# Performance work log

Hardware: AMD Instinct MI355X
Metric: run time of the kernel (lower is better)

The kernel has to match this reference:

```python
import jax, jax.numpy as jnp
import numpy as np

HEAD_SIZE = 128
B, T = 16, 2048

def setup_inputs() -> dict:
    key = jax.random.key(0)
    x = jax.random.normal(key, (B, T, 3 * HEAD_SIZE), dtype=jnp.float32)
    return {"x": x}

def reference(x) -> jnp.ndarray:
    # x: [B, T, 3*head_size] -> split into k, q, v (this order matches torch split)
    k, q, v = jnp.split(x, 3, axis=-1)  # each [B, T, D]
    d = k.shape[-1]
    scale = d ** -0.5
    # scores: [B, T, T]
    wei = jnp.einsum('bqd,bkd->bqk', q, k) * scale
    Tq = x.shape[1]
    causal = jnp.tril(jnp.ones((Tq, Tq), dtype=bool))
    wei = jnp.where(causal, wei, -jnp.inf)
    wei = jax.nn.softmax(wei, axis=-1)
    out = jnp.einsum('bqk,bkd->bqd', wei, v)  # [B, T, D]
    return out
```

## Files before the change

### kernel.cpp

```cpp
#include <hip/hip_runtime.h>

#define SEQ_T 2048
#define HDIM  128
#define NB    16
#define NTILES (SEQ_T / 64)
#define TILE_SHORTS 8192

typedef __attribute__((ext_vector_type(8))) short short8;
typedef __attribute__((ext_vector_type(4))) float float4v;
typedef __attribute__((ext_vector_type(4))) unsigned int uint4v;

#define EXP2F(x) __builtin_amdgcn_exp2f(x)

__device__ __forceinline__ unsigned int bfpack2(float a, float b) {
  unsigned int ua = __builtin_bit_cast(unsigned int, a);
  unsigned int ub = __builtin_bit_cast(unsigned int, b);
  return ((ua + 0x8000u) >> 16) | ((ub + 0x8000u) & 0xFFFF0000u);
}
__device__ __forceinline__ unsigned short f2bf(float a) {
  return (unsigned short)((__builtin_bit_cast(unsigned int, a) + 0x8000u) >> 16);
}
__device__ __forceinline__ float bf2f(unsigned short h) {
  unsigned int u = ((unsigned int)h) << 16;
  return __builtin_bit_cast(float, u);
}

__device__ __forceinline__ float dpp_max16(float x) {
  int t;
  t = __builtin_amdgcn_mov_dpp(__builtin_bit_cast(int, x), 0xB1, 0xF, 0xF, true);
  x = fmaxf(x, __builtin_bit_cast(float, t));
  t = __builtin_amdgcn_mov_dpp(__builtin_bit_cast(int, x), 0x4E, 0xF, 0xF, true);
  x = fmaxf(x, __builtin_bit_cast(float, t));
  t = __builtin_amdgcn_mov_dpp(__builtin_bit_cast(int, x), 0x141, 0xF, 0xF, true);
  x = fmaxf(x, __builtin_bit_cast(float, t));
  t = __builtin_amdgcn_mov_dpp(__builtin_bit_cast(int, x), 0x140, 0xF, 0xF, true);
  x = fmaxf(x, __builtin_bit_cast(float, t));
  return x;
}
__device__ __forceinline__ float dpp_sum16(float x) {
  int t;
  t = __builtin_amdgcn_mov_dpp(__builtin_bit_cast(int, x), 0xB1, 0xF, 0xF, true);
  x += __builtin_bit_cast(float, t);
  t = __builtin_amdgcn_mov_dpp(__builtin_bit_cast(int, x), 0x4E, 0xF, 0xF, true);
  x += __builtin_bit_cast(float, t);
  t = __builtin_amdgcn_mov_dpp(__builtin_bit_cast(int, x), 0x141, 0xF, 0xF, true);
  x += __builtin_bit_cast(float, t);
  t = __builtin_amdgcn_mov_dpp(__builtin_bit_cast(int, x), 0x140, 0xF, 0xF, true);
  x += __builtin_bit_cast(float, t);
  return x;
}

template<int CS> struct ChunkCfg;
template<> struct ChunkCfg<4> { static const int CPB = 72, SPB = 70, QB0 = 2; };
template<> struct ChunkCfg<8> { static const int CPB = 40, SPB = 36, QB0 = 4; };

__global__ __launch_bounds__(256) void prepass2(const float* __restrict__ x,
                                                unsigned short* __restrict__ kbuf,
                                                unsigned short* __restrict__ vbuf) {
  const int b = blockIdx.x >> 5;
  const int t = blockIdx.x & 31;
  const int tid = threadIdx.x;
  __shared__ __align__(16) unsigned short Klds[8192];
  __shared__ __align__(16) unsigned short Vlds[8192];

  const float* xb = x + (size_t)b * (SEQ_T * 384) + (size_t)t * 64 * 384;

  for (int i = 0; i < 8; ++i) {
    int idx = tid + i * 256;
    int row = idx >> 5, c4 = (idx & 31) << 2;
    float4v f = *(const float4v*)(xb + (size_t)row * 384 + c4);
    *(uint2*)&Klds[row * 128 + c4] = make_uint2(bfpack2(f[0], f[1]), bfpack2(f[2], f[3]));
  }
  {
    int kb = tid >> 5, db = tid & 31;
    for (int p = 0; p < 2; ++p) {
      int kbx = kb + p * 8;
      const float* vb = xb + (size_t)(4 * kbx) * 384 + 256 + 4 * db;
      float4v v0 = *(const float4v*)(vb);
      float4v v1 = *(const float4v*)(vb + 384);
      float4v v2 = *(const float4v*)(vb + 768);
      float4v v3 = *(const float4v*)(vb + 1152);
      int u = kbx >> 1, o = (kbx & 1) * 4;
      for (int j = 0; j < 4; ++j) {
        int d = 4 * db + j;
        *(uint2*)&Vlds[d * 64 + ((u + d) & 7) * 8 + o] =
            make_uint2(bfpack2(v0[j], v1[j]), bfpack2(v2[j], v3[j]));
      }
    }
  }
  __syncthreads();

  unsigned short* kdst = kbuf + (size_t)blockIdx.x * TILE_SHORTS;
  unsigned short* vdst = vbuf + (size_t)blockIdx.x * TILE_SHORTS;
  for (int i = 0; i < 4; ++i) {
    int n = tid + i * 256;
    int r = n >> 4, pu = n & 15, u = (pu - r) & 15;
    *(uint4v*)&kdst[n * 8] = *(const uint4v*)&Klds[r * 128 + u * 8];
    *(uint4v*)&vdst[n * 8] = *(const uint4v*)&Vlds[n * 8];
  }
}

template<int CS>
__global__ __launch_bounds__(512, 4) void attn_chunk_k(const float* __restrict__ x,
                                                       const unsigned short* __restrict__ kbuf,
                                                       const unsigned short* __restrict__ vbuf,
                                                       unsigned short* __restrict__ Opart,
                                                       float* __restrict__ mlpart,
                                                       float* __restrict__ out) {
  const int f = blockIdx.x;
  const int b = f / ChunkCfg<CS>::CPB;
  const int c = f - b * ChunkCfg<CS>::CPB;
  int qb = 0, cum = 0;
  for (;;) {
    int gg = (2 * qb + 2 + CS - 1) / CS;
    if (c < cum + gg) break;
    cum += gg; ++qb;
  }
  const int g = (2 * qb + 2 + CS - 1) / CS;
  const int k = c - cum;
  const int sBeg = k * CS;
  const int sEnd = min(sBeg + CS, 2 * qb + 2);

  const int tid  = threadIdx.x;
  const int qt   = tid >> 6;
  const int lane = tid & 63;
  const int low  = lane & 15;
  const int quad = lane >> 4;
  const int q0   = qb * 128 + qt * 16;

  __shared__ __align__(16) unsigned char smem[40960];
  unsigned short* Ks = (unsigned short*)smem;
  unsigned short* Vt = (unsigned short*)(smem + 16384);
  unsigned short* Ps = (unsigned short*)(smem + 32768);

  const float* xb = x + (size_t)b * (SEQ_T * 3 * HDIM);
  const unsigned short* kt = kbuf + (size_t)b * NTILES * TILE_SHORTS;
  const unsigned short* vt = vbuf + (size_t)b * NTILES * TILE_SHORTS;

  const float qs = 0.08838834764831845f * 1.4426950408889634f;
  short8 qa[4];
  {
    const float* qrow = xb + (size_t)(q0 + low) * 384 + 128;
    for (int kc = 0; kc < 4; ++kc) {
      float4v f0 = *(const float4v*)(qrow + kc * 32 + quad * 8);
      float4v f1 = *(const float4v*)(qrow + kc * 32 + quad * 8 + 4);
      uint4v u = { bfpack2(f0[0] * qs, f0[1] * qs), bfpack2(f0[2] * qs, f0[3] * qs),
                   bfpack2(f1[0] * qs, f1[1] * qs), bfpack2(f1[2] * qs, f1[3] * qs) };
      qa[kc] = __builtin_bit_cast(short8, u);
    }
  }

  float4v accv[8];
  for (int i = 0; i < 8; ++i) accv[i] = (float4v){0.f, 0.f, 0.f, 0.f};
  float l_i[4] = {0.f, 0.f, 0.f, 0.f};

  const int ch = qt * 2;

  uint4v kr0, kr1, vr0, vr1;
  {
    const unsigned short* ksrc = kt + (size_t)sBeg * TILE_SHORTS;
    const unsigned short* vsrc = vt + (size_t)sBeg * TILE_SHORTS;
    kr0 = *(const uint4v*)(ksrc + (size_t)ch * 512 + lane * 8);
    kr1 = *(const uint4v*)(ksrc + (size_t)(ch + 1) * 512 + lane * 8);
    vr0 = *(const uint4v*)(vsrc + (size_t)ch * 512 + lane * 8);
    vr1 = *(const uint4v*)(vsrc + (size_t)(ch + 1) * 512 + lane * 8);
  }

  for (int s = sBeg; s < sEnd; ++s) {
    __syncthreads();

    *(uint4v*)&Ks[(size_t)ch * 512 + lane * 8]       = kr0;
    *(uint4v*)&Ks[(size_t)(ch + 1) * 512 + lane * 8] = kr1;
    *(uint4v*)&Vt[(size_t)ch * 512 + lane * 8]       = vr0;
    *(uint4v*)&Vt[(size_t)(ch + 1) * 512 + lane * 8] = vr1;

    __syncthreads();

    if (s + 1 < sEnd) {
      const unsigned short* ksrc = kt + (size_t)(s + 1) * TILE_SHORTS;
      const unsigned short* vsrc = vt + (size_t)(s + 1) * TILE_SHORTS;
      kr0 = *(const uint4v*)(ksrc + (size_t)ch * 512 + lane * 8);
      kr1 = *(const uint4v*)(ksrc + (size_t)(ch + 1) * 512 + lane * 8);
      vr0 = *(const uint4v*)(vsrc + (size_t)ch * 512 + lane * 8);
      vr1 = *(const uint4v*)(vsrc + (size_t)(ch + 1) * 512 + lane * 8);
    }

    for (int h = 0; h < 2; ++h) {
      const int c0 = s * 64 + h * 32;
      if (c0 > q0 + 15) continue;
      const int Ra = (h << 5) + low;
      const int Rb = Ra + 16;
      float4v s0 = {0.f,0.f,0.f,0.f}, s1 = {0.f,0.f,0.f,0.f};
      for (int kc = 0; kc < 4; ++kc) {
        short8 kf0 = *(const short8*)&Ks[Ra * 128 + (((kc * 4 + quad) + Ra) & 15) * 8];
        short8 kf1 = *(const short8*)&Ks[Rb * 128 + (((kc * 4 + quad) + Rb) & 15) * 8];
        s0 = __builtin_amdgcn_mfma_f32_16x16x32_bf16(qa[kc], kf0, s0, 0, 0, 0);
        s1 = __builtin_amdgcn_mfma_f32_16x16x32_bf16(qa[kc], kf1, s1, 0, 0, 0);
      }
      if (c0 + 31 > q0) {
        for (int r = 0; r < 4; ++r) {
          int qrow = q0 + quad * 4 + r;
          s0[r] = (c0 + low      <= qrow) ? s0[r] : -1e30f;
          s1[r] = (c0 + 16 + low <= qrow) ? s1[r] : -1e30f;
        }
      }
      for (int r = 0; r < 4; ++r) {
        s0[r] = EXP2F(s0[r]);
        s1[r] = EXP2F(s1[r]);
      }
      for (int r = 0; r < 4; ++r) l_i[r] += s0[r] + s1[r];

      unsigned short* pw = Ps + qt * 512;
      for (int r = 0; r < 4; ++r) {
        int row = quad * 4 + r;
        pw[row * 32 + low]      = f2bf(s0[r]);
        pw[row * 32 + 16 + low] = f2bf(s1[r]);
      }
      short8 pa = *(const short8*)&pw[low * 32 + quad * 8];

      const int ub = (h << 2) + quad;
      for (int nt = 0; nt < 8; ++nt) {
        int d = nt * 16 + low;
        short8 vf = *(const short8*)&Vt[d * 64 + ((ub + d) & 7) * 8];
        accv[nt] = __builtin_amdgcn_mfma_f32_16x16x32_bf16(pa, vf, accv[nt], 0, 0, 0);
      }
    }
  }

  for (int r = 0; r < 4; ++r) l_i[r] = dpp_sum16(l_i[r]);

  if (g == 1) {
    float inv[4];
    for (int r = 0; r < 4; ++r) inv[r] = 1.f / l_i[r];
    float* ob = out + ((size_t)b * SEQ_T + q0) * HDIM;
    for (int nt = 0; nt < 8; ++nt)
      for (int r = 0; r < 4; ++r)
        ob[(size_t)(quad * 4 + r) * HDIM + nt * 16 + low] = accv[nt][r] * inv[r];
  } else {
    const int slot = b * ChunkCfg<CS>::SPB + (cum - ChunkCfg<CS>::QB0) + k;
    unsigned short* op = Opart + (size_t)slot * 16384 + (size_t)qt * 16 * 128;
    for (int nt = 0; nt < 8; ++nt)
      for (int r = 0; r < 4; ++r)
        op[(size_t)(quad * 4 + r) * 128 + nt * 16 + low] = f2bf(accv[nt][r]);
    if (low == 0) {
      float* ml = mlpart + (size_t)slot * 256;
      for (int r = 0; r < 4; ++r)
        ml[qt * 16 + quad * 4 + r] = l_i[r];
    }
  }
}

template<int CS>
__global__ __launch_bounds__(256) void merge_k(const unsigned short* __restrict__ Opart,
                                               const float* __restrict__ mlpart,
                                               float* __restrict__ out) {
  const int QB0 = ChunkCfg<CS>::QB0;
  const int rowsPB = (16 - QB0) * 128;
  const int ri  = blockIdx.x * 2 + (threadIdx.x >> 7);
  const int b   = ri / rowsPB;
  const int r2  = ri - b * rowsPB;
  const int qb  = QB0 + (r2 >> 7);
  const int row = r2 & 127;
  const int d   = threadIdx.x & 127;
  const int g   = (2 * qb + 2 + CS - 1) / CS;
  int cum = 0;
  for (int i = 0; i < qb; ++i) cum += (2 * i + 2 + CS - 1) / CS;
  const int s0 = b * ChunkCfg<CS>::SPB + cum - QB0;

  float num = 0.f, den = 0.f;
  for (int k = 0; k < g; ++k) {
    den += mlpart[(size_t)(s0 + k) * 256 + row];
    num += bf2f(Opart[(size_t)(s0 + k) * 16384 + (size_t)row * 128 + d]);
  }
  out[((size_t)b * SEQ_T + qb * 128 + row) * HDIM + d] = num / den;
}

__global__ __launch_bounds__(512, 4) void attn_fb(const float* __restrict__ x,
                                                  float* __restrict__ out) {
  const int b    = blockIdx.y;
  const int qblk = (int)gridDim.x - 1 - (int)blockIdx.x;
  const int qb0  = qblk << 6;
  const int tid  = threadIdx.x;
  const int wave = tid >> 6;
  const int lane = tid & 63;
  const int low  = lane & 15;
  const int quad = lane >> 4;
  const int qt   = wave & 3;
  const int half = wave >> 2;
  const int q0   = qb0 + (qt << 4);
  __shared__ __align__(16) unsigned char smem[48128];
  unsigned short* Ks = (unsigned short*)smem;
  unsigned short* Vt = (unsigned short*)(smem + 17408);
  unsigned short* Ps = (unsigned short*)(smem + 37888);
  float* Om = (float*)smem;
  float* Ml = (float*)(smem + 33792);
  const float* xb = x + (size_t)b * (SEQ_T * 3 * HDIM);
  const float qs = 0.08838834764831845f * 1.4426950408889634f;
  short8 qa[4];
  {
    const float* qrow = xb + (size_t)(q0 + low) * 384 + 128;
    for (int kc = 0; kc < 4; ++kc) {
      float4v f0 = *(const float4v*)(qrow + kc * 32 + quad * 8);
      float4v f1 = *(const float4v*)(qrow + kc * 32 + quad * 8 + 4);
      uint4v u = { bfpack2(f0[0] * qs, f0[1] * qs), bfpack2(f0[2] * qs, f0[3] * qs),
                   bfpack2(f1[0] * qs, f1[1] * qs), bfpack2(f1[2] * qs, f1[3] * qs) };
      qa[kc] = __builtin_bit_cast(short8, u);
    }
  }
  float4v accv[8];
  for (int i = 0; i < 8; ++i) accv[i] = (float4v){0.f, 0.f, 0.f, 0.f};
  float m_i[4] = {-1e30f, -1e30f, -1e30f, -1e30f};
  float l_i[4] = {0.f, 0.f, 0.f, 0.f};
  const int nsuper = qblk + 1;
  for (int s = 0; s < nsuper; ++s) {
    const int r0 = s << 6;
    __syncthreads();
    for (int i = 0; i < 4; ++i) {
      int f = tid + (i << 9);
      int row = f >> 5;
      int c4 = (f & 31) << 2;
      float4v kf = *(const float4v*)(xb + (size_t)(r0 + row) * 384 + c4);
      *(uint2*)&Ks[(row >> 5) * 4352 + (row & 31) * 136 + c4] =
          make_uint2(bfpack2(kf[0], kf[1]), bfpack2(kf[2], kf[3]));
    }
    {
      int kb = tid >> 5, db = tid & 31;
      int til = kb >> 3, kbl = kb & 7;
      const float* vbase = xb + (size_t)(r0 + 4 * kb) * 384 + 256 + 4 * db;
      float4v v0 = *(const float4v*)(vbase);
      float4v v1 = *(const float4v*)(vbase + 384);
      float4v v2 = *(const float4v*)(vbase + 768);
      float4v v3 = *(const float4v*)(vbase + 1152);
      unsigned short* vv = Vt + til * 5120;
      for (int j = 0; j < 4; ++j) {
        int d = 4 * db + j;
        int pb = ((kbl >> 1) + (d >> 3)) & 3;
        *(uint2*)&vv[d * 40 + pb * 8 + (kbl & 1) * 4] =
            make_uint2(bfpack2(v0[j], v1[j]), bfpack2(v2[j], v3[j]));
      }
    }
    __syncthreads();
    const int c0 = r0 + (half << 5);
    if (c0 <= q0 + 15) {
      const unsigned short* Ksp = Ks + half * 4352;
      const unsigned short* Vtp = Vt + half * 5120;
      float4v s0 = {0.f,0.f,0.f,0.f}, s1 = {0.f,0.f,0.f,0.f};
      for (int kc = 0; kc < 4; ++kc) {
        short8 kf0 = *(const short8*)&Ksp[low * 136 + kc * 32 + quad * 8];
        short8 kf1 = *(const short8*)&Ksp[(16 + low) * 136 + kc * 32 + quad * 8];
        s0 = __builtin_amdgcn_mfma_f32_16x16x32_bf16(qa[kc], kf0, s0, 0, 0, 0);
        s1 = __builtin_amdgcn_mfma_f32_16x16x32_bf16(qa[kc], kf1, s1, 0, 0, 0);
      }
      if (c0 + 31 > q0) {
        for (int r = 0; r < 4; ++r) {
          int qrow = q0 + quad * 4 + r;
          s0[r] = (c0 + low      <= qrow) ? s0[r] : -1e30f;
          s1[r] = (c0 + 16 + low <= qrow) ? s1[r] : -1e30f;
        }
      }
      float rmax[4], alpha[4];
      for (int r = 0; r < 4; ++r) rmax[r] = dpp_max16(fmaxf(s0[r], s1[r]));
      for (int r = 0; r < 4; ++r) {
        float mn = fmaxf(m_i[r], rmax[r]);
        alpha[r] = EXP2F(m_i[r] - mn);
        m_i[r] = mn;
      }
      for (int r = 0; r < 4; ++r) {
        s0[r] = EXP2F(s0[r] - m_i[r]);
        s1[r] = EXP2F(s1[r] - m_i[r]);
      }
      float rs[4];
      for (int r = 0; r < 4; ++r) rs[r] = dpp_sum16(s0[r] + s1[r]);
      for (int r = 0; r < 4; ++r) l_i[r] = l_i[r] * alpha[r] + rs[r];
      for (int nt = 0; nt < 8; ++nt)
        for (int r = 0; r < 4; ++r) accv[nt][r] *= alpha[r];
      unsigned short* pw = Ps + wave * 640;
      for (int r = 0; r < 4; ++r) {
        int row = quad * 4 + r;
        pw[row * 40 + low]      = f2bf(s0[r]);
        pw[row * 40 + 16 + low] = f2bf(s1[r]);
      }
      short8 pa = *(const short8*)&pw[low * 40 + quad * 8];
      for (int nt = 0; nt < 8; ++nt) {
        int d = nt * 16 + low;
        int pb = (quad + (d >> 3)) & 3;
        short8 vf = *(const short8*)&Vtp[d * 40 + pb * 8];
        accv[nt] = __builtin_amdgcn_mfma_f32_16x16x32_bf16(pa, vf, accv[nt], 0, 0, 0);
      }
    }
  }
  __syncthreads();
  if (half == 1) {
    float* om = Om + qt * 2112;
    for (int nt = 0; nt < 8; ++nt)
      for (int r = 0; r < 4; ++r)
        om[(quad * 4 + r) * 132 + nt * 16 + low] = accv[nt][r];
    if (low == 0) {
      for (int r = 0; r < 4; ++r) {
        Ml[qt * 32 + quad * 4 + r]      = m_i[r];
        Ml[qt * 32 + 16 + quad * 4 + r] = l_i[r];
      }
    }
  }
  __syncthreads();
  if (half == 0) {
    float aA[4], aB[4], linv[4];
    for (int r = 0; r < 4; ++r) {
      float mB = Ml[qt * 32 + quad * 4 + r];
      float lB = Ml[qt * 32 + 16 + quad * 4 + r];
      float mN = fmaxf(m_i[r], mB);
      aA[r] = EXP2F(m_i[r] - mN);
      aB[r] = EXP2F(mB - mN);
      linv[r] = 1.f / (l_i[r] * aA[r] + lB * aB[r]);
    }
    const float* om = Om + qt * 2112;
    float* ob = out + ((size_t)b * SEQ_T + q0) * HDIM;
    for (int nt = 0; nt < 8; ++nt)
      for (int r = 0; r < 4; ++r) {
        float o = accv[nt][r] * aA[r] + om[(quad * 4 + r) * 132 + nt * 16 + low] * aB[r];
        ob[(size_t)(quad * 4 + r) * HDIM + nt * 16 + low] = o * linv[r];
      }
  }
}

extern "C" void kernel_launch(void* const* d_in, const int* in_sizes, int n_in,
                              void* d_out, int out_size, void* d_ws, size_t ws_size,
                              hipStream_t stream) {
  const float* x = (const float*)d_in[0];
  float* out = (float*)d_out;
  const size_t PRE = (size_t)NB * NTILES * TILE_SHORTS * 2 * sizeof(unsigned short);

  const size_t OP4 = (size_t)NB * 70 * 16384 * sizeof(unsigned short);
  const size_t ML4 = (size_t)NB * 70 * 256 * sizeof(float);
  const size_t OP8 = (size_t)NB * 36 * 16384 * sizeof(unsigned short);
  const size_t ML8 = (size_t)NB * 36 * 256 * sizeof(float);

  unsigned short* kbuf = (unsigned short*)d_ws;
  unsigned short* vbuf = kbuf + (size_t)NB * NTILES * TILE_SHORTS;

  if (ws_size >= PRE + OP4 + ML4) {
    unsigned short* Opart = (unsigned short*)((char*)d_ws + PRE);
    float*          mlp   = (float*)((char*)d_ws + PRE + OP4);
    hipLaunchKernelGGL(prepass2, dim3(NB * NTILES), dim3(256), 0, stream, x, kbuf, vbuf);
    hipLaunchKernelGGL((attn_chunk_k<4>), dim3(NB * 72), dim3(512), 0, stream,
                       x, kbuf, vbuf, Opart, mlp, out);
    hipLaunchKernelGGL((merge_k<4>), dim3(NB * 14 * 128 / 2), dim3(256), 0, stream,
                       Opart, mlp, out);
  } else if (ws_size >= PRE + OP8 + ML8) {
    unsigned short* Opart = (unsigned short*)((char*)d_ws + PRE);
    float*          mlp   = (float*)((char*)d_ws + PRE + OP8);
    hipLaunchKernelGGL(prepass2, dim3(NB * NTILES), dim3(256), 0, stream, x, kbuf, vbuf);
    hipLaunchKernelGGL((attn_chunk_k<8>), dim3(NB * 40), dim3(512), 0, stream,
                       x, kbuf, vbuf, Opart, mlp, out);
    hipLaunchKernelGGL((merge_k<8>), dim3(NB * 12 * 128 / 2), dim3(256), 0, stream,
                       Opart, mlp, out);
  } else {
    hipLaunchKernelGGL(attn_fb, dim3(SEQ_T / 64, NB), dim3(512), 0, stream, x, out);
  }
}
```

Before: 143.3 us.

## Compute transposed S so P feeds PV MFMA from registers without LDS

The QK^T MFMA operands are swapped so each lane holds scores for one query row across keys, which lets the bf16 probabilities be packed straight into the A operand of the PV MFMA. This removes the per-tile LDS write and read of P (and the 8KB P buffer), with the row-sum becoming a single per-lane accumulator reduced by shuffles. To match the new key ordering, V fragments are now assembled from two 8-byte LDS reads instead of one 16-byte read, which doubles the LDS load instructions for V.

After: 147.9 us. 1.03x slower.

```diff
diff --git a/kernel.cpp b/kernel.cpp
--- a/kernel.cpp
+++ b/kernel.cpp
@@ -128,10 +128,9 @@
   const int quad = lane >> 4;
   const int q0   = qb * 128 + qt * 16;
 
-  __shared__ __align__(16) unsigned char smem[40960];
+  __shared__ __align__(16) unsigned char smem[32768];
   unsigned short* Ks = (unsigned short*)smem;
   unsigned short* Vt = (unsigned short*)(smem + 16384);
-  unsigned short* Ps = (unsigned short*)(smem + 32768);
 
   const float* xb = x + (size_t)b * (SEQ_T * 3 * HDIM);
   const unsigned short* kt = kbuf + (size_t)b * NTILES * TILE_SHORTS;
@@ -152,7 +151,7 @@
 
   float4v accv[8];
   for (int i = 0; i < 8; ++i) accv[i] = (float4v){0.f, 0.f, 0.f, 0.f};
-  float l_i[4] = {0.f, 0.f, 0.f, 0.f};
+  float l = 0.f;
 
   const int ch = qt * 2;
 
@@ -194,44 +193,48 @@
       for (int kc = 0; kc < 4; ++kc) {
         short8 kf0 = *(const short8*)&Ks[Ra * 128 + (((kc * 4 + quad) + Ra) & 15) * 8];
         short8 kf1 = *(const short8*)&Ks[Rb * 128 + (((kc * 4 + quad) + Rb) & 15) * 8];
-        s0 = __builtin_amdgcn_mfma_f32_16x16x32_bf16(qa[kc], kf0, s0, 0, 0, 0);
-        s1 = __builtin_amdgcn_mfma_f32_16x16x32_bf16(qa[kc], kf1, s1, 0, 0, 0);
+        s0 = __builtin_amdgcn_mfma_f32_16x16x32_bf16(kf0, qa[kc], s0, 0, 0, 0);
+        s1 = __builtin_amdgcn_mfma_f32_16x16x32_bf16(kf1, qa[kc], s1, 0, 0, 0);
       }
       if (c0 + 31 > q0) {
+        const int qrow = q0 + low;
         for (int r = 0; r < 4; ++r) {
-          int qrow = q0 + quad * 4 + r;
-          s0[r] = (c0 + low      <= qrow) ? s0[r] : -1e30f;
-          s1[r] = (c0 + 16 + low <= qrow) ? s1[r] : -1e30f;
+          s0[r] = (c0 + quad * 4 + r      <= qrow) ? s0[r] : -1e30f;
+          s1[r] = (c0 + 16 + quad * 4 + r <= qrow) ? s1[r] : -1e30f;
         }
       }
       for (int r = 0; r < 4; ++r) {
         s0[r] = EXP2F(s0[r]);
         s1[r] = EXP2F(s1[r]);
       }
-      for (int r = 0; r < 4; ++r) l_i[r] += s0[r] + s1[r];
-
-      unsigned short* pw = Ps + qt * 512;
-      for (int r = 0; r < 4; ++r) {
-        int row = quad * 4 + r;
-        pw[row * 32 + low]      = f2bf(s0[r]);
-        pw[row * 32 + 16 + low] = f2bf(s1[r]);
-      }
-      short8 pa = *(const short8*)&pw[low * 32 + quad * 8];
-
-      const int ub = (h << 2) + quad;
+      l += (s0[0] + s0[1]) + (s0[2] + s0[3]) + (s1[0] + s1[1]) + (s1[2] + s1[3]);
+
+      uint4v pu = { bfpack2(s0[0], s0[1]), bfpack2(s0[2], s0[3]),
+                    bfpack2(s1[0], s1[1]), bfpack2(s1[2], s1[3]) };
+      short8 pa = __builtin_bit_cast(short8, pu);
+
+      const int u0 = (h << 2) + (quad >> 1);
+      const int u1 = u0 + 2;
+      const int o4 = (quad & 1) * 4;
       for (int nt = 0; nt < 8; ++nt) {
         int d = nt * 16 + low;
-        short8 vf = *(const short8*)&Vt[d * 64 + ((ub + d) & 7) * 8];
+        uint2 va = *(const uint2*)&Vt[d * 64 + ((u0 + d) & 7) * 8 + o4];
+        uint2 vb = *(const uint2*)&Vt[d * 64 + ((u1 + d) & 7) * 8 + o4];
+        uint4v vv = { va.x, va.y, vb.x, vb.y };
+        short8 vf = __builtin_bit_cast(short8, vv);
         accv[nt] = __builtin_amdgcn_mfma_f32_16x16x32_bf16(pa, vf, accv[nt], 0, 0, 0);
       }
     }
   }
 
-  for (int r = 0; r < 4; ++r) l_i[r] = dpp_sum16(l_i[r]);
+  l += __shfl_xor(l, 16);
+  l += __shfl_xor(l, 32);
+  float lr[4];
+  for (int r = 0; r < 4; ++r) lr[r] = __shfl(l, quad * 4 + r);
 
   if (g == 1) {
     float inv[4];
-    for (int r = 0; r < 4; ++r) inv[r] = 1.f / l_i[r];
+    for (int r = 0; r < 4; ++r) inv[r] = 1.f / lr[r];
     float* ob = out + ((size_t)b * SEQ_T + q0) * HDIM;
     for (int nt = 0; nt < 8; ++nt)
       for (int r = 0; r < 4; ++r)
@@ -245,7 +248,7 @@
     if (low == 0) {
       float* ml = mlpart + (size_t)slot * 256;
       for (int r = 0; r < 4; ++r)
-        ml[qt * 16 + quad * 4 + r] = l_i[r];
+        ml[qt * 16 + quad * 4 + r] = lr[r];
     }
   }
 }
```
